# Performance work log

Hardware: AMD Instinct MI355X
Metric: run time of the kernel (lower is better)

Reference implementation:

```python
import jax, jax.numpy as jnp
import numpy as np

FAR = 10.0
RAST = 256          # rast_size default
ORIG_W, ORIG_H = 256.0, 256.0  # orig_size default
CHUNK = 32          # faces processed per scan step
EPS = 1e-9


def _project(vertices, K, R, t, dist):
    # persp projection with lens distortion; vertices [B,V,3] -> [B,V,3] (u,v in [-1,1], z depth)
    v = jnp.einsum('bvj,bij->bvi', vertices, R) + t
    x, y, z = v[..., 0], v[..., 1], v[..., 2]
    x_ = x / (z + EPS)
    y_ = y / (z + EPS)
    k1, k2, p1, p2, k3 = (dist[:, None, i] for i in range(5))
    r2 = x_ * x_ + y_ * y_  # == r**2 in original (r = sqrt(x_^2+y_^2))
    radial = 1.0 + k1 * r2 + k2 * r2 ** 2 + k3 * r2 ** 3
    x__ = x_ * radial + 2.0 * p1 * x_ * y_ + p2 * (r2 + 2.0 * x_ ** 2)
    y__ = y_ * radial + p1 * (r2 + 2.0 * y_ ** 2) + 2.0 * p2 * x_ * y_
    pts = jnp.stack([x__, y__, jnp.ones_like(z)], axis=-1)
    pts = jnp.einsum('bvj,bij->bvi', pts, K)
    u, vv = pts[..., 0], pts[..., 1]
    vv = ORIG_H - vv
    u = 2.0 * (u - ORIG_W / 2.0) / ORIG_W
    vv = 2.0 * (vv - ORIG_H / 2.0) / ORIG_H
    return jnp.stack([u, vv, z], axis=-1)


def _rasterize(fverts):
    # fverts: [B,F,3,3] per-face screen-space vertices (u,v,z). Z-buffer depth raster + coverage mask.
    B, F = fverts.shape[0], fverts.shape[1]
    pad = (-F) % CHUNK
    fv = jnp.pad(fverts, ((0, 0), (0, pad), (0, 0), (0, 0)))  # padded faces are degenerate (den==0)
    nc = (F + pad) // CHUNK
    fv = fv.reshape(B, nc, CHUNK, 3, 3).transpose(1, 0, 2, 3, 4)  # [nc,B,CHUNK,3,3]
    # pixel centers in [-1,1]; row i top-to-bottom maps to y = -1..1 (consistent with flipped v)
    g = 2.0 * (jnp.arange(RAST, dtype=jnp.float32) + 0.5) / RAST - 1.0
    X = g[None, None, None, :]   # cols
    Y = g[None, None, :, None]   # rows

    def body(carry, ch):
        zbuf, cover = carry
        e = lambda i, j: ch[:, :, i, j][:, :, None, None]
        ax, ay, az = e(0, 0), e(0, 1), e(0, 2)
        bx, by, bz = e(1, 0), e(1, 1), e(1, 2)
        cx, cy, cz = e(2, 0), e(2, 1), e(2, 2)
        den = (bx - ax) * (cy - ay) - (by - ay) * (cx - ax)
        ok = jnp.abs(den) > 1e-8
        den_s = jnp.where(ok, den, 1.0)
        # barycentric coords of each pixel wrt this face (signed; fill_back provides both windings)
        w0 = ((by - cy) * (X - cx) + (cx - bx) * (Y - cy)) / den_s
        w1 = ((cy - ay) * (X - cx) + (ax - cx) * (Y - cy)) / den_s
        w2 = 1.0 - w0 - w1
        zs = lambda zz: jnp.where(zz > 1e-8, zz, 1.0)
        inv = w0 / zs(az) + w1 / zs(bz) + w2 / zs(cz)  # perspective-correct 1/z interp
        valid = ok & (w0 >= 0) & (w1 >= 0) & (w2 >= 0)
        valid = valid & (az > 1e-8) & (bz > 1e-8) & (cz > 1e-8) & (inv > 1e-8)
        zp = 1.0 / jnp.where(valid, inv, 1.0)
        zc = jnp.min(jnp.where(valid, zp, FAR), axis=1)  # nearest face in this chunk [B,S,S]
        return (jnp.minimum(zbuf, zc), cover | jnp.any(valid, axis=1)), None

    zbuf0 = jnp.full((B, RAST, RAST), FAR, dtype=jnp.float32)
    cov0 = jnp.zeros((B, RAST, RAST), dtype=bool)
    (zbuf, cover), _ = jax.lax.scan(body, (zbuf0, cov0), fv)
    return zbuf, cover


def _normalize_depth(img, far):
    img_inf = (img == far).astype(jnp.float32)
    img_no_back = (1.0 - img_inf) * img
    img_max = img_no_back.max(axis=1, keepdims=True).max(axis=2, keepdims=True)
    img_min = img.min(axis=1, keepdims=True).min(axis=2, keepdims=True)
    nd = (img_max - img) / (img_max - img_min + 1e-4)
    return jnp.clip(nd, 0.0, 1.0)


def _forward(vertices, faces, intr, R, t, dist_coeffs):
    # fill_back=True: append faces with reversed vertex order
    faces_fb = jnp.concatenate([faces, faces[:, :, ::-1]], axis=1)
    uvz = _project(vertices, intr, R, t, dist_coeffs)
    fverts = jax.vmap(lambda v, f: v[f])(uvz, faces_fb)  # [B,F,3,3]
    zbuf, cover = _rasterize(fverts)
    dep = _normalize_depth(zbuf, FAR)
    mask = cover.astype(jnp.float32)
    return dep, mask


def setup_inputs():
    key = jax.random.key(0)
    k0, k1, k2 = jax.random.split(key, 3)
    B, V, F = 4, 778, 1538  # MANO hand mesh
    vertices = jax.random.normal(k0, (B, V, 3), dtype=jnp.float32) * 0.1 \
        + jnp.array([0.0, 0.0, 0.6], dtype=jnp.float32)  # blob 0.6m in front of camera
    faces = jax.random.randint(k1, (B, F, 3), 0, V, dtype=jnp.int32)
    K = jnp.tile(jnp.array([[500.0, 0.0, 128.0],
                            [0.0, 500.0, 128.0],
                            [0.0, 0.0, 1.0]], dtype=jnp.float32)[None], (B, 1, 1))
    R = jnp.tile(jnp.eye(3, dtype=jnp.float32)[None], (B, 1, 1))
    t = jnp.zeros((B, 1, 3), dtype=jnp.float32)
    dist_coeffs = jax.random.uniform(k2, (B, 5), dtype=jnp.float32) * 0.01
    return {"vertices": vertices, "faces": faces, "intr": K, "R": R, "t": t,
            "dist_coeffs": dist_coeffs}


def reference(vertices, faces, intr, R, t, dist_coeffs):
    return _forward(vertices, faces, intr, R, t, dist_coeffs)
```

## Files before the change

kernel.cpp:

```cpp
#include <hip/hip_runtime.h>
#include <cstdint>

#define RASTN 256
#define FARV 10.0f
#define FARBITS 0x41200000u
#define SPLIT 4
#define NBUCK 1024
#define NINITY 8

__device__ __forceinline__ float gval(int i) {
    return (2.0f * ((float)i + 0.5f)) / 256.0f - 1.0f;
}

__global__ __launch_bounds__(1024) void prep_sort_kernel(
    const float* __restrict__ verts, const int* __restrict__ faces,
    const float* __restrict__ Km, const float* __restrict__ Rm,
    const float* __restrict__ tm, const float* __restrict__ dm,
    float4* __restrict__ rec, uint2* __restrict__ sax, unsigned short* __restrict__ stri,
    unsigned int* __restrict__ zbits, unsigned int* __restrict__ mm,
    float* __restrict__ uvzg, int V, int F, int F2, int B, int npix)
{
#pragma clang fp contract(off)
    __shared__ float s_uvz[1024*3];
    __shared__ unsigned int s_pk[4096];
    __shared__ unsigned short s_bk[4096];
    __shared__ unsigned int s_hist[NBUCK], s_cnt2[NBUCK];
    __shared__ unsigned int s_ws[16];
    int b = blockIdx.x, y = blockIdx.y, tid = threadIdx.x;
    int lane = tid & 63, wv16 = tid >> 6;
    uint4* zb4 = (uint4*)(zbits + (size_t)b * npix);
    int n4 = npix >> 2;
    int sl0 = (n4 * y) / NINITY, sl1 = (n4 * (y + 1)) / NINITY;
    for (int i = sl0 + tid; i < sl1; i += 1024)
        zb4[i] = make_uint4(FARBITS, FARBITS, FARBITS, FARBITS);
    if (y > 0) return;
    if (tid == 0) { mm[2*b] = 0u; mm[2*b+1] = FARBITS; }
    for (int i = tid; i < NBUCK; i += 1024) s_hist[i] = 0u;
    bool inlds = (V <= 1024);
    const float* R = Rm + b*9; const float* K = Km + b*9;
    const float* t = tm + b*3; const float* d = dm + b*5;
    for (int v = tid; v < V; v += 1024) {
        float vx = verts[((size_t)b*V + v)*3+0];
        float vy = verts[((size_t)b*V + v)*3+1];
        float vz = verts[((size_t)b*V + v)*3+2];
        float cxm = ((vx*R[0] + vy*R[1]) + vz*R[2]) + t[0];
        float cym = ((vx*R[3] + vy*R[4]) + vz*R[5]) + t[1];
        float czm = ((vx*R[6] + vy*R[7]) + vz*R[8]) + t[2];
        float zd = czm + 1e-9f;
        float x_ = cxm / zd;
        float y_ = cym / zd;
        float k1 = d[0], k2 = d[1], p1 = d[2], p2 = d[3], k3 = d[4];
        float r2   = (x_*x_) + (y_*y_);
        float r2_2 = r2 * r2;
        float r2_3 = r2 * r2_2;
        float radial = ((1.0f + k1*r2) + k2*r2_2) + k3*r2_3;
        float x__ = ((x_*radial) + (((2.0f*p1)*x_)*y_)) + (p2*(r2 + 2.0f*(x_*x_)));
        float y__ = ((y_*radial) + (p1*(r2 + 2.0f*(y_*y_)))) + (((2.0f*p2)*x_)*y_);
        float up = ((x__*K[0]) + (y__*K[1])) + (1.0f*K[2]);
        float vp = ((x__*K[3]) + (y__*K[4])) + (1.0f*K[5]);
        vp = 256.0f - vp;
        float un = (2.0f*(up - 128.0f)) / 256.0f;
        float vn = (2.0f*(vp - 128.0f)) / 256.0f;
        if (inlds) { s_uvz[v*3+0]=un; s_uvz[v*3+1]=vn; s_uvz[v*3+2]=czm; }
        else { uvzg[((size_t)b*V+v)*3+0]=un; uvzg[((size_t)b*V+v)*3+1]=vn; uvzg[((size_t)b*V+v)*3+2]=czm; }
    }
    __syncthreads();
    const float* ub = inlds ? s_uvz : (uvzg + (size_t)b*V*3);
    const int* fb = faces + (size_t)b * F * 3;
    float4* rb = rec + (size_t)b * F2 * 4;
    bool stash = (F2 <= 4096);
    for (int j = tid; j < F2; j += 1024) {
        int i0, i1, i2;
        if (j < F) { i0 = fb[j*3+0]; i1 = fb[j*3+1]; i2 = fb[j*3+2]; }
        else { int jj = j - F; i0 = fb[jj*3+2]; i1 = fb[jj*3+1]; i2 = fb[jj*3+0]; }
        float ax = ub[i0*3+0], ay = ub[i0*3+1], az = ub[i0*3+2];
        float bx = ub[i1*3+0], by = ub[i1*3+1], bz = ub[i1*3+2];
        float cx = ub[i2*3+0], cy = ub[i2*3+1], cz = ub[i2*3+2];
        float den = (bx-ax)*(cy-ay) - (by-ay)*(cx-ax);
        bool ok = fabsf(den) > 1e-8f;
        float dens = ok ? den : 1.0f;
        bool alive = ok && (az > 1e-8f) && (bz > 1e-8f) && (cz > 1e-8f);
        float za = (az > 1e-8f) ? az : 1.0f;
        float zb = (bz > 1e-8f) ? bz : 1.0f;
        float zc = (cz > 1e-8f) ? cz : 1.0f;
        float mnx = fminf(ax, fminf(bx, cx));
        float mxx = fmaxf(ax, fmaxf(bx, cx));
        float mny = fminf(ay, fminf(by, cy));
        float mxy = fmaxf(ay, fmaxf(by, cy));
        float m = 1e-3f + 1e-6f*((fabsf(mnx)+fabsf(mxx))+(fabsf(mny)+fabsf(mxy)));
        mnx -= m; mxx += m; mny -= m; mxy += m;
        if (!(mxx >= -1.0f) || !(mnx <= 1.0f) || !(mxy >= -1.0f) || !(mny <= 1.0f)) alive = false;
        int ic0 = 1, ic1 = 0, ir0 = 1, ir1 = 0;
        float minz = 3e38f;
        if (alive) {
            float lx = fmaxf(mnx, -1.5f), hx = fminf(mxx, 1.5f);
            float ly = fmaxf(mny, -1.5f), hy = fminf(mxy, 1.5f);
            ic0 = (int)floorf((lx + 1.0f) * 128.0f - 0.5f);
            ic1 = (int)ceilf ((hx + 1.0f) * 128.0f - 0.5f);
            ir0 = (int)floorf((ly + 1.0f) * 128.0f - 0.5f);
            ir1 = (int)ceilf ((hy + 1.0f) * 128.0f - 0.5f);
            ic0 = ic0 < 0 ? 0 : ic0;  ir0 = ir0 < 0 ? 0 : ir0;
            ic1 = ic1 > 255 ? 255 : ic1;  ir1 = ir1 > 255 ? 255 : ir1;
            if (ic0 > ic1 || ir0 > ir1) { ic0 = 1; ic1 = 0; ir0 = 1; ir1 = 0; minz = 3e38f; }
            else minz = fminf(za, fminf(zb, zc)) * (1.0f - 4e-4f);
        }
        float minzv = fminf(za, fminf(zb, zc));
        float maxzv = fmaxf(za, fmaxf(zb, zc));
        float a0 = by - cy, b0 = cx - bx;
        float a1 = cy - ay, b1 = ax - cx;
        float densf = dens;
        if (dens < 0.0f) { a0 = -a0; b0 = -b0; a1 = -a1; b1 = -b1; densf = -dens; }
        float rd = __builtin_amdgcn_rcpf(densf);
        float ra, rbz, rc;
        if (minzv > 1e-2f && maxzv < 100.0f * minzv) {
            ra  = __builtin_amdgcn_rcpf(za);
            rbz = __builtin_amdgcn_rcpf(zb);
            rc  = __builtin_amdgcn_rcpf(zc);
        } else {
            ra = rbz = rc = __builtin_huge_valf();
        }
        unsigned int pack = (unsigned int)(ic0 | (ic1 << 8) | (ir0 << 16) | (ir1 << 24));
        int bk = NBUCK - 1;
        if (minz < 1e30f) {
            bk = (int)(minz * 512.0f);
            bk = bk < 0 ? 0 : (bk > NBUCK-2 ? NBUCK-2 : bk);
        }
        size_t base = (size_t)j * 4;
        rb[base+0] = make_float4(cx, cy, a0, b0);
        rb[base+1] = make_float4(a1, b1, rd, ra);
        rb[base+2] = make_float4(densf, za, zb, zc);
        rb[base+3] = make_float4(__uint_as_float(pack), minz, rbz, rc);
        atomicAdd(&s_hist[bk], 1u);
        if (stash) { s_pk[j] = pack; s_bk[j] = (unsigned short)bk; }
    }
    __syncthreads();
    {
        unsigned int h = s_hist[tid];
        unsigned int v = h;
        for (int o = 1; o < 64; o <<= 1) {
            unsigned int tsh = __shfl_up(v, o, 64);
            if (lane >= o) v += tsh;
        }
        if (lane == 63) s_ws[wv16] = v;
        __syncthreads();
        if (tid < 16) {
            unsigned int w = s_ws[tid];
            for (int o = 1; o < 16; o <<= 1) {
                unsigned int tsh = __shfl_up(w, o, 64);
                if (tid >= o) w += tsh;
            }
            s_ws[tid] = w;
        }
        __syncthreads();
        unsigned int add = (wv16 > 0) ? s_ws[wv16 - 1] : 0u;
        s_cnt2[tid] = v + add - h;
    }
    __syncthreads();
    uint2* sxb = sax + (size_t)b * F2;
    unsigned short* stb = stri + (size_t)b * F2;
    for (int j = tid; j < F2; j += 1024) {
        unsigned int pack; int bk;
        if (stash) { pack = s_pk[j]; bk = (int)s_bk[j]; }
        else {
            float4 q3 = rb[(size_t)j*4+3];
            pack = __float_as_uint(q3.x);
            float mz = q3.y;
            bk = NBUCK - 1;
            if (mz < 1e30f) { bk = (int)(mz * 512.0f); bk = bk < 0 ? 0 : (bk > NBUCK-2 ? NBUCK-2 : bk); }
        }
        float key = (bk == NBUCK-1) ? 3e38f : (float)bk * (1.0f/512.0f);
        int pos = (int)atomicAdd(&s_cnt2[bk], 1u);
        sxb[pos] = make_uint2(pack, __float_as_uint(key));
        stb[pos] = (unsigned short)j;
    }
}

__global__ __launch_bounds__(256) void raster_kernel(
    const float4* __restrict__ rec, const uint2* __restrict__ sax,
    const unsigned short* __restrict__ stri, unsigned int* __restrict__ zbits,
    int F2)
{
#pragma clang fp contract(off)
    __shared__ float4 sh[256];
    __shared__ float2 s_kb[256];
    __shared__ unsigned short s_list[256];
    __shared__ int s_wk[4], s_kk[4], s_wo[4];
    __shared__ int s_tot, s_kc;
    __shared__ float s_tzmax, s_red[4];
    int zz = blockIdx.z;
    int b = zz / SPLIT, sp = zz - b*SPLIT;
    int tc = blockIdx.x, tr = blockIdx.y;
    int tid = threadIdx.x, lane = tid & 63, wv = tid >> 6;
    int tx = tid & 15, ty = tid >> 4;
    int col = tc*16 + tx, row = tr*16 + ty;
    float X = gval(col), Y = gval(row);
    int pc0 = tc*16, pc1 = pc0+15, pr0 = tr*16, pr1 = pr0+15;
    int wvs = __builtin_amdgcn_readfirstlane(wv);
    int wr0 = pr0 + wvs*4, wr1 = wr0 + 3;
    float Xc = 0.5f*(gval(pc0) + gval(pc1));
    float Yc = 0.5f*(gval(pr0) + gval(pr1));
    const float hxr = 15.0f/256.0f, hyr = 15.0f/256.0f;
    const float4* rb = rec + (size_t)b * F2 * 4;
    const uint2* sxb = sax + (size_t)b * F2;
    const unsigned short* stb = stri + (size_t)b * F2;
    size_t pix = ((size_t)b*RASTN + row)*RASTN + col;
    unsigned int* zp_g = zbits + pix;
    float zmin = FARV;
    float pushed = FARV;
    if (tid == 0) s_tzmax = FARV;
    __syncthreads();
    int nch = (F2 + 256*SPLIT - 1) / (256*SPLIT);
    for (int c = 0; c < nch; ++c) {
        int s = (c*256 + tid)*SPLIT + sp;
        bool kp = false, sv = false; unsigned int tri = 0; float kf = 0.0f;
        unsigned int pkv = 0;
        if (s < F2) {
            uint2 a = sxb[s];
            kf = __uint_as_float(a.y);
            kp = !(kf > s_tzmax);
            if (kp) {
                int pk = (int)a.x;
                int ic0 = pk & 255, ic1 = (pk >> 8) & 255;
                int ir0 = (pk >> 16) & 255, ir1 = (pk >> 24) & 255;
                sv = (ic0 <= ic1) && (ic0 <= pc1) && (ic1 >= pc0) && (ir0 <= pr1) && (ir1 >= pr0);
                if (sv) {
                    tri = stb[s];
                    pkv = a.x;
                    float4 q0 = rb[(size_t)tri*4 + 0];
                    float4 q1 = rb[(size_t)tri*4 + 1];
                    float4 q2 = rb[(size_t)tri*4 + 2];
                    float a0 = q0.z, b0 = q0.w;
                    float a1 = q1.x, b1 = q1.y;
                    float xcd = Xc - q0.x, ycd = Yc - q0.y;
                    float e0c = (a0*xcd) + (b0*ycd);
                    float e1c = (a1*xcd) + (b1*ycd);
                    float den = q2.x;
                    float e2c = (den - e0c) - e1c;
                    float a2 = -(a0 + a1), b2 = -(b0 + b1);
                    float t0 = fabsf(a0)*hxr + fabsf(b0)*hyr;
                    float t1 = fabsf(a1)*hxr + fabsf(b1)*hyr;
                    float t2 = fabsf(a2)*hxr + fabsf(b2)*hyr;
                    float m0 = e0c + t0;
                    float m1 = e1c + t1;
                    float m2 = e2c + t2;
                    bool cull = (m0 < -1e-5f*(fabsf(e0c) + t0 + 1.0f))
                             || (m1 < -1e-5f*(fabsf(e1c) + t1 + 1.0f))
                             || (m2 < -1e-5f*(fabsf(e2c) + t2 + 1.0f));
                    if (cull) sv = false;
                }
            }
        }
        unsigned long long bs = __ballot(sv ? 1 : 0);
        unsigned long long bk = __ballot(kp ? 1 : 0);
        int pfx = __popcll(bs & ((1ull << lane) - 1ull));
        if (lane == 0) { s_wk[wv] = __popcll(bs); s_kk[wv] = __popcll(bk); }
        __syncthreads();
        if (tid == 0) {
            int acc = 0;
            for (int q = 0; q < 4; ++q) { s_wo[q] = acc; acc += s_wk[q]; }
            s_tot = acc;
            s_kc = s_kk[0] + s_kk[1] + s_kk[2] + s_kk[3];
        }
        __syncthreads();
        if (sv) {
            int pos = s_wo[wv] + pfx;
            s_list[pos] = (unsigned short)tri;
            s_kb[pos] = make_float2(kf, __uint_as_float(pkv));
        }
        int kcnt = s_kc, n = s_tot;
        if (kcnt == 0) break;
        for (int g = 0; g < n; g += 64) {
            __syncthreads();
            float zg = __uint_as_float(__hip_atomic_load(
                zp_g, __ATOMIC_RELAXED, __HIP_MEMORY_SCOPE_AGENT));
            float2 kbv = s_kb[g + lane];
            int cnt2 = (n - g) < 64 ? (n - g) : 64;
            if (tid < cnt2*4) {
                unsigned int t4 = s_list[g + (tid >> 2)];
                sh[tid] = rb[(size_t)t4*4 + (tid & 3)];
            }
            __syncthreads();
            pushed = fminf(pushed, zg);
            zmin = fminf(zmin, zg);
            int vkey = __float_as_int(kbv.x);
            int vbb  = __float_as_int(kbv.y);
            for (int i = 0; i < cnt2; ++i) {
                float ky = __int_as_float(__builtin_amdgcn_readlane(vkey, i));
                if (ky > zmin) break;
                unsigned int pk = (unsigned int)__builtin_amdgcn_readlane(vbb, i);
                int ir0 = (int)((pk >> 16) & 255u), ir1 = (int)(pk >> 24);
                if (ir1 < wr0 || ir0 > wr1) continue;
                int ic0 = (int)(pk & 255u), ic1 = (int)((pk >> 8) & 255u);
                if (col < ic0 || col > ic1 || row < ir0 || row > ir1) continue;
                float4 q0 = sh[i*4+0];
                float4 q1 = sh[i*4+1];
                float xc = X - q0.x;
                float yc = Y - q0.y;
                float e0 = (q0.z*xc) + (q0.w*yc);
                float e1 = (q1.x*xc) + (q1.y*yc);
                float rd = q1.z;
                float w0a = e0*rd, w1a = e1*rd;
                float w2a = (1.0f - w0a) - w1a;
                float epsu = 1e-4f*((1.0f + fabsf(w0a)) + fabsf(w1a));
                if (e0 > -1e-30f && e1 > -1e-30f && w2a > -epsu) {
                    float4 q3 = sh[i*4+3];
                    float inva = ((w0a*q1.w) + (w1a*q3.z)) + (w2a*q3.w);
                    float zpa = __builtin_amdgcn_rcpf(inva);
                    bool clearly = (e0 > 0.0f) && (e1 > 0.0f) && (w2a > epsu) && (inva > 1e-6f);
                    if (!clearly || zpa < zmin*1.001f) {
                        float4 q2 = sh[i*4+2];
                        float dens = q2.x;
                        float w0 = e0 / dens;
                        float w1 = e1 / dens;
                        float w2 = (1.0f - w0) - w1;
                        float inv = ((w0 / q2.y) + (w1 / q2.z)) + (w2 / q2.w);
                        if ((w0 >= 0.0f) && (w1 >= 0.0f) && (w2 >= 0.0f) && (inv > 1e-8f)) {
                            float zp = 1.0f / inv;
                            zmin = fminf(zmin, zp);
                        }
                    }
                }
            }
            if (zmin < pushed) {
                atomicMin(zp_g, __float_as_uint(zmin));
                pushed = zmin;
            }
        }
        if (n > 0) {
            float zx = zmin;
            for (int o = 32; o; o >>= 1) zx = fmaxf(zx, __shfl_xor(zx, o));
            if (lane == 0) s_red[wv] = zx;
        }
        __syncthreads();
        if (n > 0 && tid == 0)
            s_tzmax = fminf(s_tzmax,
                fmaxf(fmaxf(s_red[0], s_red[1]), fmaxf(s_red[2], s_red[3])));
        __syncthreads();
    }
    if (zmin < pushed)
        atomicMin(zp_g, __float_as_uint(zmin));
}

__global__ __launch_bounds__(256) void minmax_kernel(
    const float4* __restrict__ zbuf, float4* __restrict__ mask,
    unsigned int* __restrict__ mm, int npix)
{
    __shared__ float smx[4], smn[4];
    int b = blockIdx.y;
    size_t i4 = (((size_t)b * npix) >> 2) + (size_t)blockIdx.x * 256 + threadIdx.x;
    float4 z = zbuf[i4];
    float4 mk;
    mk.x = (z.x < FARV) ? 1.0f : 0.0f;
    mk.y = (z.y < FARV) ? 1.0f : 0.0f;
    mk.z = (z.z < FARV) ? 1.0f : 0.0f;
    mk.w = (z.w < FARV) ? 1.0f : 0.0f;
    mask[i4] = mk;
    float nbx = (z.x == FARV) ? 0.0f : z.x;
    float nby = (z.y == FARV) ? 0.0f : z.y;
    float nbz = (z.z == FARV) ? 0.0f : z.z;
    float nbw = (z.w == FARV) ? 0.0f : z.w;
    float vmx = fmaxf(fmaxf(nbx, nby), fmaxf(nbz, nbw));
    float vmn = fminf(fminf(z.x, z.y), fminf(z.z, z.w));
    int lane = threadIdx.x & 63, wv = threadIdx.x >> 6;
    for (int o = 32; o; o >>= 1) {
        vmx = fmaxf(vmx, __shfl_xor(vmx, o));
        vmn = fminf(vmn, __shfl_xor(vmn, o));
    }
    if (lane == 0) { smx[wv] = vmx; smn[wv] = vmn; }
    __syncthreads();
    if (threadIdx.x == 0) {
        float bmx = fmaxf(fmaxf(smx[0], smx[1]), fmaxf(smx[2], smx[3]));
        float bmn = fminf(fminf(smn[0], smn[1]), fminf(smn[2], smn[3]));
        atomicMax(mm + 2*b,     __float_as_uint(bmx));
        atomicMin(mm + 2*b + 1, __float_as_uint(bmn));
    }
}

__global__ __launch_bounds__(256) void final_kernel(
    float4* __restrict__ zdep, const unsigned int* __restrict__ mm,
    int npix4, int total4)
{
#pragma clang fp contract(off)
    int idx = blockIdx.x*256 + threadIdx.x;
    if (idx >= total4) return;
    int b = idx / npix4;
    float mx = __uint_as_float(mm[2*b]);
    float mn = __uint_as_float(mm[2*b + 1]);
    float den = (mx - mn) + 1e-4f;
    float4 z = zdep[idx];
    float4 r;
    r.x = (mx - z.x) / den;
    r.y = (mx - z.y) / den;
    r.z = (mx - z.z) / den;
    r.w = (mx - z.w) / den;
    r.x = r.x < 0.0f ? 0.0f : (r.x > 1.0f ? 1.0f : r.x);
    r.y = r.y < 0.0f ? 0.0f : (r.y > 1.0f ? 1.0f : r.y);
    r.z = r.z < 0.0f ? 0.0f : (r.z > 1.0f ? 1.0f : r.z);
    r.w = r.w < 0.0f ? 0.0f : (r.w > 1.0f ? 1.0f : r.w);
    zdep[idx] = r;
}

extern "C" void kernel_launch(void* const* d_in, const int* in_sizes, int n_in,
                              void* d_out, int out_size, void* d_ws, size_t ws_size,
                              hipStream_t stream)
{
    const float* verts = (const float*)d_in[0];
    const int*   faces = (const int*)d_in[1];
    const float* Km    = (const float*)d_in[2];
    const float* Rm    = (const float*)d_in[3];
    const float* tm    = (const float*)d_in[4];
    const float* dm    = (const float*)d_in[5];
    float* out = (float*)d_out;

    int B  = in_sizes[2] / 9;
    int V  = in_sizes[0] / (3 * B);
    int F  = in_sizes[1] / (3 * B);
    int F2 = 2 * F;
    int npix = RASTN * RASTN;

    char* ws = (char*)d_ws;
    size_t off = 0;
    float4* rec = (float4*)(ws + off);
    off = (off + (size_t)B * F2 * 4 * sizeof(float4) + 255) & ~(size_t)255;
    uint2* sax = (uint2*)(ws + off);
    off = (off + (size_t)B * F2 * sizeof(uint2) + 255) & ~(size_t)255;
    unsigned short* stri = (unsigned short*)(ws + off);
    off = (off + (size_t)B * F2 * sizeof(unsigned short) + 255) & ~(size_t)255;
    float* uvzg = (float*)(ws + off);
    off = (off + (size_t)B * V * 3 * sizeof(float) + 255) & ~(size_t)255;
    unsigned int* mm = (unsigned int*)(ws + off);

    unsigned int* zbits = (unsigned int*)out;
    float* mask = out + (size_t)B * npix;

    dim3 pgrid(B, NINITY);
    prep_sort_kernel<<<pgrid, 1024, 0, stream>>>(
        verts, faces, Km, Rm, tm, dm, rec, sax, stri, zbits, mm, uvzg,
        V, F, F2, B, npix);
    dim3 rgrid(16, 16, B * SPLIT);
    raster_kernel<<<rgrid, 256, 0, stream>>>(rec, sax, stri, zbits, F2);
    dim3 mgrid(npix / 1024, B);
    minmax_kernel<<<mgrid, 256, 0, stream>>>(
        (const float4*)zbits, (float4*)mask, mm, npix);
    int npix4 = npix >> 2;
    int total4 = B * npix4;
    final_kernel<<<(total4 + 255) / 256, 256, 0, stream>>>(
        (float4*)zbits, mm, npix4, total4);
}
```

Measured before the change: 160.6 us.

## Deinterleave sorted face list per split and repack face record fields

The sorted face keys and indices are now written in a split-major layout, so each raster split reads a contiguous segment instead of a stride-SPLIT gather. Padding entries with a far key fill the tail. The per-face record fields are also reordered so the setup path reads only the first two float4s (density moves into q1), and the fast depth test uses q2 instead of q3. The aim is coalesced list loads and one fewer global load per candidate face, at the cost of a modulo and divide per scatter in the sort.

```diff
diff --git a/kernel.cpp b/kernel.cpp
--- a/kernel.cpp
+++ b/kernel.cpp
@@ -18,7 +18,7 @@
     const float* __restrict__ tm, const float* __restrict__ dm,
     float4* __restrict__ rec, uint2* __restrict__ sax, unsigned short* __restrict__ stri,
     unsigned int* __restrict__ zbits, unsigned int* __restrict__ mm,
-    float* __restrict__ uvzg, int V, int F, int F2, int B, int npix)
+    float* __restrict__ uvzg, int V, int F, int F2, int F2c, int B, int npix)
 {
 #pragma clang fp contract(off)
     __shared__ float s_uvz[1024*3];
@@ -36,6 +36,14 @@
     if (y > 0) return;
     if (tid == 0) { mm[2*b] = 0u; mm[2*b+1] = FARBITS; }
     for (int i = tid; i < NBUCK; i += 1024) s_hist[i] = 0u;
+    int seg = F2c / SPLIT;
+    uint2* sxb = sax + (size_t)b * F2c;
+    unsigned short* stb = stri + (size_t)b * F2c;
+    for (int p = F2 + tid; p < F2c; p += 1024) {
+        int addr = (p % SPLIT) * seg + p / SPLIT;
+        sxb[addr] = make_uint2(1u , __float_as_uint(3e38f));
+        stb[addr] = 0;
+    }
     bool inlds = (V <= 1024);
     const float* R = Rm + b*9; const float* K = Km + b*9;
     const float* t = tm + b*3; const float* d = dm + b*5;
@@ -127,9 +135,9 @@
         }
         size_t base = (size_t)j * 4;
         rb[base+0] = make_float4(cx, cy, a0, b0);
-        rb[base+1] = make_float4(a1, b1, rd, ra);
-        rb[base+2] = make_float4(densf, za, zb, zc);
-        rb[base+3] = make_float4(__uint_as_float(pack), minz, rbz, rc);
+        rb[base+1] = make_float4(a1, b1, densf, rd);
+        rb[base+2] = make_float4(ra, rbz, rc, minz);
+        rb[base+3] = make_float4(__uint_as_float(pack), za, zb, zc);
         atomicAdd(&s_hist[bk], 1u);
         if (stash) { s_pk[j] = pack; s_bk[j] = (unsigned short)bk; }
     }
@@ -156,29 +164,29 @@
         s_cnt2[tid] = v + add - h;
     }
     __syncthreads();
-    uint2* sxb = sax + (size_t)b * F2;
-    unsigned short* stb = stri + (size_t)b * F2;
     for (int j = tid; j < F2; j += 1024) {
         unsigned int pack; int bk;
         if (stash) { pack = s_pk[j]; bk = (int)s_bk[j]; }
         else {
             float4 q3 = rb[(size_t)j*4+3];
+            float4 q2 = rb[(size_t)j*4+2];
             pack = __float_as_uint(q3.x);
-            float mz = q3.y;
+            float mz = q2.w;
             bk = NBUCK - 1;
             if (mz < 1e30f) { bk = (int)(mz * 512.0f); bk = bk < 0 ? 0 : (bk > NBUCK-2 ? NBUCK-2 : bk); }
         }
         float key = (bk == NBUCK-1) ? 3e38f : (float)bk * (1.0f/512.0f);
         int pos = (int)atomicAdd(&s_cnt2[bk], 1u);
-        sxb[pos] = make_uint2(pack, __float_as_uint(key));
-        stb[pos] = (unsigned short)j;
+        int addr = (pos % SPLIT) * seg + pos / SPLIT;
+        sxb[addr] = make_uint2(pack, __float_as_uint(key));
+        stb[addr] = (unsigned short)j;
     }
 }
 
 __global__ __launch_bounds__(256) void raster_kernel(
     const float4* __restrict__ rec, const uint2* __restrict__ sax,
     const unsigned short* __restrict__ stri, unsigned int* __restrict__ zbits,
-    int F2)
+    int F2, int F2c)
 {
 #pragma clang fp contract(off)
     __shared__ float4 sh[256];
@@ -200,21 +208,22 @@
     float Xc = 0.5f*(gval(pc0) + gval(pc1));
     float Yc = 0.5f*(gval(pr0) + gval(pr1));
     const float hxr = 15.0f/256.0f, hyr = 15.0f/256.0f;
+    int seg = F2c / SPLIT;
     const float4* rb = rec + (size_t)b * F2 * 4;
-    const uint2* sxb = sax + (size_t)b * F2;
-    const unsigned short* stb = stri + (size_t)b * F2;
+    const uint2* sxb = sax + (size_t)b * F2c + (size_t)sp * seg;
+    const unsigned short* stb = stri + (size_t)b * F2c + (size_t)sp * seg;
     size_t pix = ((size_t)b*RASTN + row)*RASTN + col;
     unsigned int* zp_g = zbits + pix;
     float zmin = FARV;
     float pushed = FARV;
     if (tid == 0) s_tzmax = FARV;
     __syncthreads();
-    int nch = (F2 + 256*SPLIT - 1) / (256*SPLIT);
+    int nch = (seg + 255) / 256;
     for (int c = 0; c < nch; ++c) {
-        int s = (c*256 + tid)*SPLIT + sp;
+        int s = c*256 + tid;
         bool kp = false, sv = false; unsigned int tri = 0; float kf = 0.0f;
         unsigned int pkv = 0;
-        if (s < F2) {
+        if (s < seg) {
             uint2 a = sxb[s];
             kf = __uint_as_float(a.y);
             kp = !(kf > s_tzmax);
@@ -228,13 +237,12 @@
                     pkv = a.x;
                     float4 q0 = rb[(size_t)tri*4 + 0];
                     float4 q1 = rb[(size_t)tri*4 + 1];
-                    float4 q2 = rb[(size_t)tri*4 + 2];
                     float a0 = q0.z, b0 = q0.w;
                     float a1 = q1.x, b1 = q1.y;
                     float xcd = Xc - q0.x, ycd = Yc - q0.y;
                     float e0c = (a0*xcd) + (b0*ycd);
                     float e1c = (a1*xcd) + (b1*ycd);
-                    float den = q2.x;
+                    float den = q1.z;
                     float e2c = (den - e0c) - e1c;
                     float a2 = -(a0 + a1), b2 = -(b0 + b1);
                     float t0 = fabsf(a0)*hxr + fabsf(b0)*hyr;
@@ -298,22 +306,22 @@
                 float yc = Y - q0.y;
                 float e0 = (q0.z*xc) + (q0.w*yc);
                 float e1 = (q1.x*xc) + (q1.y*yc);
-                float rd = q1.z;
+                float rd = q1.w;
                 float w0a = e0*rd, w1a = e1*rd;
                 float w2a = (1.0f - w0a) - w1a;
                 float epsu = 1e-4f*((1.0f + fabsf(w0a)) + fabsf(w1a));
                 if (e0 > -1e-30f && e1 > -1e-30f && w2a > -epsu) {
-                    float4 q3 = sh[i*4+3];
-                    float inva = ((w0a*q1.w) + (w1a*q3.z)) + (w2a*q3.w);
+                    float4 q2 = sh[i*4+2];
+                    float inva = ((w0a*q2.x) + (w1a*q2.y)) + (w2a*q2.z);
                     float zpa = __builtin_amdgcn_rcpf(inva);
                     bool clearly = (e0 > 0.0f) && (e1 > 0.0f) && (w2a > epsu) && (inva > 1e-6f);
                     if (!clearly || zpa < zmin*1.001f) {
-                        float4 q2 = sh[i*4+2];
-                        float dens = q2.x;
+                        float4 q3 = sh[i*4+3];
+                        float dens = q1.z;
                         float w0 = e0 / dens;
                         float w1 = e1 / dens;
                         float w2 = (1.0f - w0) - w1;
-                        float inv = ((w0 / q2.y) + (w1 / q2.z)) + (w2 / q2.w);
+                        float inv = ((w0 / q3.y) + (w1 / q3.z)) + (w2 / q3.w);
                         if ((w0 >= 0.0f) && (w1 >= 0.0f) && (w2 >= 0.0f) && (inv > 1e-8f)) {
                             float zp = 1.0f / inv;
                             zmin = fminf(zmin, zp);
@@ -416,6 +424,7 @@
     int V  = in_sizes[0] / (3 * B);
     int F  = in_sizes[1] / (3 * B);
     int F2 = 2 * F;
+    int F2c = ((F2 + SPLIT - 1) / SPLIT) * SPLIT;
     int npix = RASTN * RASTN;
 
     char* ws = (char*)d_ws;
@@ -423,9 +432,9 @@
     float4* rec = (float4*)(ws + off);
     off = (off + (size_t)B * F2 * 4 * sizeof(float4) + 255) & ~(size_t)255;
     uint2* sax = (uint2*)(ws + off);
-    off = (off + (size_t)B * F2 * sizeof(uint2) + 255) & ~(size_t)255;
+    off = (off + (size_t)B * F2c * sizeof(uint2) + 255) & ~(size_t)255;
     unsigned short* stri = (unsigned short*)(ws + off);
-    off = (off + (size_t)B * F2 * sizeof(unsigned short) + 255) & ~(size_t)255;
+    off = (off + (size_t)B * F2c * sizeof(unsigned short) + 255) & ~(size_t)255;
     float* uvzg = (float*)(ws + off);
     off = (off + (size_t)B * V * 3 * sizeof(float) + 255) & ~(size_t)255;
     unsigned int* mm = (unsigned int*)(ws + off);
@@ -436,9 +445,9 @@
     dim3 pgrid(B, NINITY);
     prep_sort_kernel<<<pgrid, 1024, 0, stream>>>(
         verts, faces, Km, Rm, tm, dm, rec, sax, stri, zbits, mm, uvzg,
-        V, F, F2, B, npix);
+        V, F, F2, F2c, B, npix);
     dim3 rgrid(16, 16, B * SPLIT);
-    raster_kernel<<<rgrid, 256, 0, stream>>>(rec, sax, stri, zbits, F2);
+    raster_kernel<<<rgrid, 256, 0, stream>>>(rec, sax, stri, zbits, F2, F2c);
     dim3 mgrid(npix / 1024, B);
     minmax_kernel<<<mgrid, 256, 0, stream>>>(
         (const float4*)zbits, (float4*)mask, mm, npix);
```

Result: no change. 160.7 us (+0.1%).
